# Optimization experiments

Measured on AMD Instinct MI355X. Metric: run time of the kernel, lower is better.

The kernel has to match this reference:

```python
import jax, jax.numpy as jnp
import numpy as np

K = 3  # kernel size
PAD = K // 2


def setup_inputs() -> dict:
    key = jax.random.key(0)
    k1, k2, k3 = jax.random.split(key, 3)
    B, C, H, W = 8, 192, 128, 128
    x = jax.random.normal(k1, (B, C, H, W), dtype=jnp.float32)
    kernel = 0.02 * jax.random.normal(k2, (C, K * K), dtype=jnp.float32)
    gate_w = 0.02 * jax.random.normal(k3, (C,), dtype=jnp.float32)
    gate_b = jnp.zeros((C,), dtype=jnp.float32)
    return {"x": x, "kernel": kernel, "gate_w": gate_w, "gate_b": gate_b}


def reference(x, kernel, gate_w, gate_b):
    B, C, H, W = x.shape
    # F.unfold with zero padding: patches[b,c,ki*K+kj,h,w] = x_pad[b,c,h+ki,w+kj]
    xp = jnp.pad(x, ((0, 0), (0, 0), (PAD, PAD), (PAD, PAD)))
    patches = jnp.stack(
        [xp[:, :, i:i + H, j:j + W] for i in range(K) for j in range(K)],
        axis=2,
    )  # [B, C, K*K, H, W]
    # depthwise 1x1 gate: per-channel scale + bias, then sigmoid
    theta = jax.nn.sigmoid(x * gate_w[None, :, None, None] + gate_b[None, :, None, None])
    # max-plus: max_v [ f(u-v) + theta(u) * k(v) ]
    scored = patches + theta[:, :, None] * kernel[None, :, :, None, None]
    return jnp.max(scored, axis=2)  # [B, C, H, W]
```

## Files before the change

kernel.cpp:

```cpp
#include <hip/hip_runtime.h>
#include <math.h>

#define BB 8
#define CC 192
#define HH 128
#define WW 128
#define RPT 8

typedef float vf4 __attribute__((ext_vector_type(4)));

__device__ __forceinline__ float col9(float a0, float a1, float a2,
                                      float b0, float b1, float b2,
                                      float c0, float c1, float c2,
                                      float th, const float* kk) {
    float m;
    m = fmaf(th, kk[0], a0);
    m = fmaxf(m, fmaf(th, kk[1], a1));
    m = fmaxf(m, fmaf(th, kk[2], a2));
    m = fmaxf(m, fmaf(th, kk[3], b0));
    m = fmaxf(m, fmaf(th, kk[4], b1));
    m = fmaxf(m, fmaf(th, kk[5], b2));
    m = fmaxf(m, fmaf(th, kk[6], c0));
    m = fmaxf(m, fmaf(th, kk[7], c1));
    m = fmaxf(m, fmaf(th, kk[8], c2));
    return m;
}

__global__ __launch_bounds__(256) void dynmorph_kernel(
    const float* __restrict__ x,
    const float* __restrict__ kern,
    const float* __restrict__ gw,
    const float* __restrict__ gb,
    float* __restrict__ out)
{
    const int tid  = threadIdx.x;
    const int lane = tid & 63;
    const int wg   = lane & 31;
    const int rs   = (tid >> 6) * 2 + (lane >> 5);
    const int col  = wg * 4;
    const int r0   = blockIdx.y * (RPT * 8) + rs * RPT;

    const int bc = blockIdx.x;
    const int c  = bc % CC;

    const float* xp = x   + (size_t)bc * (HH * WW);
    float*       op = out + (size_t)bc * (HH * WW);

    float kk[9];
#pragma unroll
    for (int i = 0; i < 9; ++i) kk[i] = kern[c * 9 + i];
    const float gwc = gw[c];
    const float gbc = gb[c];

    vf4 v[RPT + 2];
#pragma unroll
    for (int i = 0; i < RPT + 2; ++i) {
        const int g = r0 - 1 + i;
        if (g >= 0 && g < HH) {
            v[i] = *(const vf4*)(xp + g * WW + col);
        } else {
            v[i] = (vf4)(0.0f);
        }
    }
    __builtin_amdgcn_sched_barrier(0);

    float lf[RPT + 2], rt[RPT + 2];
#pragma unroll
    for (int i = 0; i < RPT + 2; ++i) {
        const float l = __shfl_up(v[i].w, 1);
        const float r = __shfl_down(v[i].x, 1);
        lf[i] = (wg == 0)  ? 0.0f : l;
        rt[i] = (wg == 31) ? 0.0f : r;
    }
    __builtin_amdgcn_sched_barrier(0);

#pragma unroll
    for (int g = 0; g < RPT; ++g) {
        const vf4 A = v[g], B = v[g + 1], Cv = v[g + 2];

        const float t0 = __builtin_amdgcn_rcpf(1.0f + __expf(-fmaf(B.x, gwc, gbc)));
        const float t1 = __builtin_amdgcn_rcpf(1.0f + __expf(-fmaf(B.y, gwc, gbc)));
        const float t2 = __builtin_amdgcn_rcpf(1.0f + __expf(-fmaf(B.z, gwc, gbc)));
        const float t3 = __builtin_amdgcn_rcpf(1.0f + __expf(-fmaf(B.w, gwc, gbc)));

        vf4 o;
        o.x = col9(lf[g],   A.x, A.y,
                   lf[g+1], B.x, B.y,
                   lf[g+2], Cv.x, Cv.y, t0, kk);
        o.y = col9(A.x, A.y, A.z,
                   B.x, B.y, B.z,
                   Cv.x, Cv.y, Cv.z, t1, kk);
        o.z = col9(A.y, A.z, A.w,
                   B.y, B.z, B.w,
                   Cv.y, Cv.z, Cv.w, t2, kk);
        o.w = col9(A.z, A.w, rt[g],
                   B.z, B.w, rt[g+1],
                   Cv.z, Cv.w, rt[g+2], t3, kk);

        __builtin_nontemporal_store(o, (vf4*)(op + (r0 + g) * WW + col));
    }
}

extern "C" void kernel_launch(void* const* d_in, const int* in_sizes, int n_in,
                              void* d_out, int out_size, void* d_ws, size_t ws_size,
                              hipStream_t stream) {
    const float* x    = (const float*)d_in[0];
    const float* kern = (const float*)d_in[1];
    const float* gw   = (const float*)d_in[2];
    const float* gb   = (const float*)d_in[3];
    float* out        = (float*)d_out;

    dim3 grid(BB * CC, 2);
    dim3 block(256);
    dynmorph_kernel<<<grid, block, 0, stream>>>(x, kern, gw, gb, out);
}
```

Before: 187.5 us.

## Process a whole plane per block with a rolling prefetch buffer of rows

Each block now covers a full 128-row channel plane instead of half of one, so each thread handles 16 rows. Rows are loaded through a 7-entry rolling register buffer with a prefetch distance of 6, so loads overlap with the max-plus compute instead of all being issued up front. This halves the grid and reduces halo reloads between row slabs. The cost is fewer blocks for latency hiding and reliance on the compiler keeping the rotating buffer in registers.

```diff
diff --git a/kernel.cpp b/kernel.cpp
--- a/kernel.cpp
+++ b/kernel.cpp
@@ -5,7 +5,9 @@
 #define CC 192
 #define HH 128
 #define WW 128
-#define RPT 8
+#define RPS 16
+#define DPF 6
+#define NB  (DPF + 1)
 
 typedef float vf4 __attribute__((ext_vector_type(4)));
 
@@ -38,7 +40,7 @@
     const int wg   = lane & 31;
     const int rs   = (tid >> 6) * 2 + (lane >> 5);
     const int col  = wg * 4;
-    const int r0   = blockIdx.y * (RPT * 8) + rs * RPT;
+    const int r0   = rs * RPS;
 
     const int bc = blockIdx.x;
     const int c  = bc % CC;
@@ -52,31 +54,46 @@
     const float gwc = gw[c];
     const float gbc = gb[c];
 
-    vf4 v[RPT + 2];
+    auto ld = [&](int i) -> vf4 {
+        const int g = r0 - 1 + i;
+        if (g >= 0 && g < HH) return *(const vf4*)(xp + g * WW + col);
+        return (vf4)(0.0f);
+    };
+
+    vf4   buf[NB];
+    float lfh[RPS + 2], rth[RPS + 2];
+
 #pragma unroll
-    for (int i = 0; i < RPT + 2; ++i) {
-        const int g = r0 - 1 + i;
-        if (g >= 0 && g < HH) {
-            v[i] = *(const vf4*)(xp + g * WW + col);
-        } else {
-            v[i] = (vf4)(0.0f);
-        }
-    }
-    __builtin_amdgcn_sched_barrier(0);
-
-    float lf[RPT + 2], rt[RPT + 2];
-#pragma unroll
-    for (int i = 0; i < RPT + 2; ++i) {
-        const float l = __shfl_up(v[i].w, 1);
-        const float r = __shfl_down(v[i].x, 1);
-        lf[i] = (wg == 0)  ? 0.0f : l;
-        rt[i] = (wg == 31) ? 0.0f : r;
-    }
+    for (int i = 0; i < DPF; ++i) buf[i % NB] = ld(i);
     __builtin_amdgcn_sched_barrier(0);
 
 #pragma unroll
-    for (int g = 0; g < RPT; ++g) {
-        const vf4 A = v[g], B = v[g + 1], Cv = v[g + 2];
+    for (int i = 0; i < 2; ++i) {
+        const vf4 t = buf[i % NB];
+        const float l = __shfl_up(t.w, 1);
+        const float r = __shfl_down(t.x, 1);
+        lfh[i] = (wg == 0)  ? 0.0f : l;
+        rth[i] = (wg == 31) ? 0.0f : r;
+    }
+
+#pragma unroll
+    for (int g = 0; g < RPS; ++g) {
+        if (g + DPF < RPS + 2) {
+            buf[(g + DPF) % NB] = ld(g + DPF);
+        }
+        __builtin_amdgcn_sched_barrier(0);
+
+        {
+            const vf4 t = buf[(g + 2) % NB];
+            const float l = __shfl_up(t.w, 1);
+            const float r = __shfl_down(t.x, 1);
+            lfh[g + 2] = (wg == 0)  ? 0.0f : l;
+            rth[g + 2] = (wg == 31) ? 0.0f : r;
+        }
+
+        const vf4 A  = buf[g % NB];
+        const vf4 B  = buf[(g + 1) % NB];
+        const vf4 Cv = buf[(g + 2) % NB];
 
         const float t0 = __builtin_amdgcn_rcpf(1.0f + __expf(-fmaf(B.x, gwc, gbc)));
         const float t1 = __builtin_amdgcn_rcpf(1.0f + __expf(-fmaf(B.y, gwc, gbc)));
@@ -84,18 +101,18 @@
         const float t3 = __builtin_amdgcn_rcpf(1.0f + __expf(-fmaf(B.w, gwc, gbc)));
 
         vf4 o;
-        o.x = col9(lf[g],   A.x, A.y,
-                   lf[g+1], B.x, B.y,
-                   lf[g+2], Cv.x, Cv.y, t0, kk);
+        o.x = col9(lfh[g],   A.x, A.y,
+                   lfh[g+1], B.x, B.y,
+                   lfh[g+2], Cv.x, Cv.y, t0, kk);
         o.y = col9(A.x, A.y, A.z,
                    B.x, B.y, B.z,
                    Cv.x, Cv.y, Cv.z, t1, kk);
         o.z = col9(A.y, A.z, A.w,
                    B.y, B.z, B.w,
                    Cv.y, Cv.z, Cv.w, t2, kk);
-        o.w = col9(A.z, A.w, rt[g],
-                   B.z, B.w, rt[g+1],
-                   Cv.z, Cv.w, rt[g+2], t3, kk);
+        o.w = col9(A.z, A.w, rth[g],
+                   B.z, B.w, rth[g+1],
+                   Cv.z, Cv.w, rth[g+2], t3, kk);
 
         __builtin_nontemporal_store(o, (vf4*)(op + (r0 + g) * WW + col));
     }
@@ -110,7 +127,7 @@
     const float* gb   = (const float*)d_in[3];
     float* out        = (float*)d_out;
 
-    dim3 grid(BB * CC, 2);
+    dim3 grid(BB * CC);
     dim3 block(256);
     dynmorph_kernel<<<grid, block, 0, stream>>>(x, kern, gw, gb, out);
 }
```

Result: no change. 184.2 us (-1.8%).

## Stream row tiles through double-buffered LDS via direct global-to-LDS loads

Applied to the files above, without the earlier changes.

Each block now covers a whole (batch, channel) plane instead of half of one. It walks eight 16-row tiles, loading each tile plus its halo rows into a double-buffered shared-memory buffer with global_load_lds. The next tile's load is issued before the current tile is computed, so loads overlap compute, and the halo overhead per tile drops. The cost is half as many blocks, a block-wide barrier per tile, and reliance on the barrier to wait for the async LDS loads to finish.

```diff
diff --git a/kernel.cpp b/kernel.cpp
--- a/kernel.cpp
+++ b/kernel.cpp
@@ -5,9 +5,19 @@
 #define CC 192
 #define HH 128
 #define WW 128
-#define RPT 8
+#define TH 16
+#define NTILE 8
+#define SLOTS 18
+#define TILE_FLOATS (SLOTS * WW)
 
 typedef float vf4 __attribute__((ext_vector_type(4)));
+
+__device__ __forceinline__ void gl_lds16(const float* g, float* l) {
+    __builtin_amdgcn_global_load_lds(
+        (const __attribute__((address_space(1))) void*)g,
+        (__attribute__((address_space(3))) void*)l,
+        16, 0, 0);
+}
 
 __device__ __forceinline__ float col9(float a0, float a1, float a2,
                                       float b0, float b1, float b2,
@@ -33,12 +43,14 @@
     const float* __restrict__ gb,
     float* __restrict__ out)
 {
+    __shared__ __attribute__((aligned(16))) float sbuf[2][TILE_FLOATS];
+
     const int tid  = threadIdx.x;
     const int lane = tid & 63;
+    const int wv   = tid >> 6;
     const int wg   = lane & 31;
-    const int rs   = (tid >> 6) * 2 + (lane >> 5);
+    const int half = lane >> 5;
     const int col  = wg * 4;
-    const int r0   = blockIdx.y * (RPT * 8) + rs * RPT;
 
     const int bc = blockIdx.x;
     const int c  = bc % CC;
@@ -52,52 +64,74 @@
     const float gwc = gw[c];
     const float gbc = gb[c];
 
-    vf4 v[RPT + 2];
+    auto issue_tile = [&](int tt) {
+        float* lb = &sbuf[tt & 1][0];
+        const int base = tt * TH - 1;
+        for (int i = wv; i < 9; i += 4) {
+            const int gr = base + 2 * i;
+            const float* g = xp + gr * WW + lane * 4;
+            float*       l = lb + i * 256;
+            if (gr >= 0 && gr + 1 < HH) {
+                gl_lds16(g, l);
+            } else if (gr < 0) {
+                if (lane >= 32) gl_lds16(g, l);
+            } else if (gr < HH) {
+                if (lane < 32) gl_lds16(g, l);
+            }
+        }
+        if (tt == 0         && tid < WW) lb[tid] = 0.0f;
+        if (tt == NTILE - 1 && tid < WW) lb[17 * WW + tid] = 0.0f;
+    };
+
+    auto compute_tile = [&](int tt) {
+        const float* lb = &sbuf[tt & 1][0];
+        const int r0 = tt * TH;
 #pragma unroll
-    for (int i = 0; i < RPT + 2; ++i) {
-        const int g = r0 - 1 + i;
-        if (g >= 0 && g < HH) {
-            v[i] = *(const vf4*)(xp + g * WW + col);
-        } else {
-            v[i] = (vf4)(0.0f);
+        for (int i = 0; i < 2; ++i) {
+            const int rr = 4 * wv + 2 * i + half;
+            const vf4 A  = *(const vf4*)(lb + (rr    ) * WW + col);
+            const vf4 B  = *(const vf4*)(lb + (rr + 1) * WW + col);
+            const vf4 Cv = *(const vf4*)(lb + (rr + 2) * WW + col);
+
+            float lA = __shfl_up(A.w, 1),  rA = __shfl_down(A.x, 1);
+            float lB = __shfl_up(B.w, 1),  rB = __shfl_down(B.x, 1);
+            float lC = __shfl_up(Cv.w, 1), rC = __shfl_down(Cv.x, 1);
+            lA = (wg == 0)  ? 0.0f : lA;
+            lB = (wg == 0)  ? 0.0f : lB;
+            lC = (wg == 0)  ? 0.0f : lC;
+            rA = (wg == 31) ? 0.0f : rA;
+            rB = (wg == 31) ? 0.0f : rB;
+            rC = (wg == 31) ? 0.0f : rC;
+
+            const float t0 = __builtin_amdgcn_rcpf(1.0f + __expf(-fmaf(B.x, gwc, gbc)));
+            const float t1 = __builtin_amdgcn_rcpf(1.0f + __expf(-fmaf(B.y, gwc, gbc)));
+            const float t2 = __builtin_amdgcn_rcpf(1.0f + __expf(-fmaf(B.z, gwc, gbc)));
+            const float t3 = __builtin_amdgcn_rcpf(1.0f + __expf(-fmaf(B.w, gwc, gbc)));
+
+            vf4 o;
+            o.x = col9(lA,  A.x, A.y,
+                       lB,  B.x, B.y,
+                       lC,  Cv.x, Cv.y, t0, kk);
+            o.y = col9(A.x, A.y, A.z,
+                       B.x, B.y, B.z,
+                       Cv.x, Cv.y, Cv.z, t1, kk);
+            o.z = col9(A.y, A.z, A.w,
+                       B.y, B.z, B.w,
+                       Cv.y, Cv.z, Cv.w, t2, kk);
+            o.w = col9(A.z, A.w, rA,
+                       B.z, B.w, rB,
+                       Cv.z, Cv.w, rC,  t3, kk);
+
+            __builtin_nontemporal_store(o, (vf4*)(op + (r0 + rr) * WW + col));
         }
-    }
-    __builtin_amdgcn_sched_barrier(0);
+    };
 
-    float lf[RPT + 2], rt[RPT + 2];
-#pragma unroll
-    for (int i = 0; i < RPT + 2; ++i) {
-        const float l = __shfl_up(v[i].w, 1);
-        const float r = __shfl_down(v[i].x, 1);
-        lf[i] = (wg == 0)  ? 0.0f : l;
-        rt[i] = (wg == 31) ? 0.0f : r;
-    }
-    __builtin_amdgcn_sched_barrier(0);
-
-#pragma unroll
-    for (int g = 0; g < RPT; ++g) {
-        const vf4 A = v[g], B = v[g + 1], Cv = v[g + 2];
-
-        const float t0 = __builtin_amdgcn_rcpf(1.0f + __expf(-fmaf(B.x, gwc, gbc)));
-        const float t1 = __builtin_amdgcn_rcpf(1.0f + __expf(-fmaf(B.y, gwc, gbc)));
-        const float t2 = __builtin_amdgcn_rcpf(1.0f + __expf(-fmaf(B.z, gwc, gbc)));
-        const float t3 = __builtin_amdgcn_rcpf(1.0f + __expf(-fmaf(B.w, gwc, gbc)));
-
-        vf4 o;
-        o.x = col9(lf[g],   A.x, A.y,
-                   lf[g+1], B.x, B.y,
-                   lf[g+2], Cv.x, Cv.y, t0, kk);
-        o.y = col9(A.x, A.y, A.z,
-                   B.x, B.y, B.z,
-                   Cv.x, Cv.y, Cv.z, t1, kk);
-        o.z = col9(A.y, A.z, A.w,
-                   B.y, B.z, B.w,
-                   Cv.y, Cv.z, Cv.w, t2, kk);
-        o.w = col9(A.z, A.w, rt[g],
-                   B.z, B.w, rt[g+1],
-                   Cv.z, Cv.w, rt[g+2], t3, kk);
-
-        __builtin_nontemporal_store(o, (vf4*)(op + (r0 + g) * WW + col));
+    issue_tile(0);
+    __syncthreads();
+    for (int tt = 0; tt < NTILE; ++tt) {
+        if (tt + 1 < NTILE) issue_tile(tt + 1);
+        compute_tile(tt);
+        __syncthreads();
     }
 }
 
@@ -110,7 +144,7 @@
     const float* gb   = (const float*)d_in[3];
     float* out        = (float*)d_out;
 
-    dim3 grid(BB * CC, 2);
+    dim3 grid(BB * CC);
     dim3 block(256);
     dynmorph_kernel<<<grid, block, 0, stream>>>(x, kern, gw, gb, out);
 }
```

Measured after the change: 184.9 us. About the same (-1.4%).
